# Kernel tuning notes

Hardware: AMD Instinct MI355X
Metric: run time of the kernel (lower is better)

Reference implementation:

```python
import jax, jax.numpy as jnp
import numpy as np

HEADS = 4
DIM_HEAD = 32


def setup_inputs() -> dict:
    key = jax.random.key(0)
    k1, k2, k3, k4 = jax.random.split(key, 4)
    dim = 128
    hidden = HEADS * DIM_HEAD  # 128
    x = jax.random.normal(k1, (32, dim, 64, 64), dtype=jnp.float32)
    w_qkv = jax.random.normal(k2, (3 * hidden, dim), dtype=jnp.float32) * (1.0 / np.sqrt(dim))
    w_out = jax.random.normal(k3, (dim, hidden), dtype=jnp.float32) * (1.0 / np.sqrt(hidden))
    b_out = jax.random.normal(k4, (dim,), dtype=jnp.float32) * 0.01
    return {"x": x, "w_qkv": w_qkv, "w_out": w_out, "b_out": b_out}


def reference(x, w_qkv, w_out, b_out):
    b, c, h, w = x.shape
    n = h * w
    # 1x1 conv (no bias) == channel matmul
    qkv = jnp.einsum('oc,bchw->bohw', w_qkv, x)  # [b, 3*heads*dh, h, w]
    qkv = qkv.reshape(b, 3, HEADS, DIM_HEAD, n)
    q, k, v = qkv[:, 0], qkv[:, 1], qkv[:, 2]  # each [b, heads, dh, n]
    k = jax.nn.softmax(k, axis=-1)  # softmax over spatial positions
    context = jnp.einsum('bhdn,bhen->bhde', k, v)  # [b, heads, dh, dh]
    out = jnp.einsum('bhde,bhdn->bhen', context, q)  # [b, heads, dh, n]
    out = out.reshape(b, HEADS * DIM_HEAD, h, w)
    # 1x1 conv with bias
    return jnp.einsum('oc,bchw->bohw', w_out, out) + b_out[None, :, None, None]
```

## Files before the change

### kernel.cpp

```cpp
#include <hip/hip_runtime.h>
#include <hip/hip_bf16.h>
#include <math.h>

#define BATCH 32
#define CDIM  128
#define NTOT  4096
#define NCH   16
#define CHN   256
#define TN    64

typedef __attribute__((ext_vector_type(4))) float f32x4;
typedef __attribute__((ext_vector_type(8))) short s16x8;

#define PC_OFF  0
#define PC_SIZE (BATCH * 4 * NCH * 32 * 32)
#define PS_OFF  (PC_OFF + PC_SIZE)
#define PS_SIZE (BATCH * 4 * NCH * 32)
#define MBF_OFF (PS_OFF + PS_SIZE)
#define MBF_SIZE (BATCH * CDIM * CDIM / 2)
#define XBT_OFF (MBF_OFF + MBF_SIZE)
#define XBT_SIZE (BATCH * CDIM * NTOT / 2)
#define NEED_BYTES ((size_t)(XBT_OFF + XBT_SIZE) * 4)

static __device__ __forceinline__ unsigned short f2bf(float f) {
    return __builtin_bit_cast(unsigned short, __float2bfloat16(f));
}
static __device__ __forceinline__ unsigned int pack2(float a, float b) {
    return (unsigned int)f2bf(a) | ((unsigned int)f2bf(b) << 16);
}
static __device__ __forceinline__ s16x8 ld_frag_lds(const unsigned int* xsd, int d0) {
    int4 t;
    t.x = (int)xsd[d0]; t.y = (int)xsd[d0 + 1];
    t.z = (int)xsd[d0 + 2]; t.w = (int)xsd[d0 + 3];
    return __builtin_bit_cast(s16x8, t);
}

static __device__ __forceinline__ void stage_xT(const float* __restrict__ xc,
                                                unsigned int* __restrict__ xsd,
                                                int tid) {
    const int m  = tid & 15;
    const int cg = tid >> 4;
#pragma unroll
    for (int p = 0; p < 4; ++p) {
        const int c = 2 * cg + 32 * p;
        const f32x4 a0 = *reinterpret_cast<const f32x4*>(xc + (size_t)c * NTOT + 4 * m);
        const f32x4 a1 = *reinterpret_cast<const f32x4*>(xc + (size_t)(c + 1) * NTOT + 4 * m);
#pragma unroll
        for (int jj = 0; jj < 4; ++jj)
            xsd[(4 * m + jj) * 65 + (c >> 1)] = pack2(a0[jj], a1[jj]);
    }
}

template <bool XBT>
__global__ __launch_bounds__(256, 2)
void k1_ctx(const float* __restrict__ x, const float* __restrict__ wqkv,
            float* __restrict__ ws) {
    __shared__ __attribute__((aligned(16))) unsigned short xsT[64 * 130];
    __shared__ __attribute__((aligned(16))) unsigned short ekv[8][32][72];

    const int j = blockIdx.x, b = blockIdx.y;
    const int tid = threadIdx.x;
    const int l = tid & 63;
    const int w = tid >> 6;
    const int m = l & 15, hq = l >> 4;

    s16x8 afr[4][4];
#pragma unroll
    for (int tm = 0; tm < 4; ++tm)
#pragma unroll
        for (int kt = 0; kt < 4; ++kt) {
            const float* wr = wqkv +
                (size_t)(CDIM + 64 * w + 16 * tm + m) * CDIM + 32 * kt + 8 * hq;
            const f32x4 u0 = *reinterpret_cast<const f32x4*>(wr);
            const f32x4 u1 = *reinterpret_cast<const f32x4*>(wr + 4);
            int4 t4;
            t4.x = (int)pack2(u0[0], u0[1]); t4.y = (int)pack2(u0[2], u0[3]);
            t4.z = (int)pack2(u1[0], u1[1]); t4.w = (int)pack2(u1[2], u1[3]);
            afr[tm][kt] = __builtin_bit_cast(s16x8, t4);
        }

    f32x4 cacc[2][2] = {};
    float sacc[4][4] = {};
    const float* xc = x + (size_t)b * CDIM * NTOT + j * CHN;
    unsigned int* xsd = (unsigned int*)xsT;

    for (int it = 0; it < CHN / TN; ++it) {
        stage_xT(xc + it * TN, xsd, tid);
        __syncthreads();

        if constexpr (XBT) {
            unsigned int* tb = (unsigned int*)(ws + XBT_OFF) +
                               ((size_t)(b * NCH + j) * 4 + it) * 4096;
            const int n = tid >> 2, qt = tid & 3;
#pragma unroll
            for (int p = 0; p < 4; ++p) {
                const int cdl = 16 * p + 4 * qt;
                const int src = n * 65 + (cdl ^ ((n & 7) << 2));
                uint4 v;
                v.x = xsd[src]; v.y = xsd[src + 1];
                v.z = xsd[src + 2]; v.w = xsd[src + 3];
                *reinterpret_cast<uint4*>(tb + (size_t)n * 64 + cdl) = v;
            }
        }

        f32x4 acc[4][4] = {};
#pragma unroll
        for (int kt = 0; kt < 4; ++kt) {
#pragma unroll
            for (int tn = 0; tn < 4; ++tn) {
                const s16x8 bfr = ld_frag_lds(xsd, (16 * tn + m) * 65 + 16 * kt + 4 * hq);
#pragma unroll
                for (int tm = 0; tm < 4; ++tm)
                    acc[tm][tn] = __builtin_amdgcn_mfma_f32_16x16x32_bf16(
                        afr[tm][kt], bfr, acc[tm][tn], 0, 0, 0);
            }
        }

        if (w < 2) {
#pragma unroll
            for (int tm = 0; tm < 4; ++tm)
#pragma unroll
                for (int tn = 0; tn < 4; ++tn)
#pragma unroll
                    for (int r = 0; r < 4; ++r) {
                        const int dg = 64 * w + 16 * tm + 4 * hq + r;
                        const float e = __expf(acc[tm][tn][r]);
                        sacc[tm][r] += e;
                        ekv[dg >> 5][dg & 31][16 * tn + m] = f2bf(e);
                    }
        } else {
#pragma unroll
            for (int tm = 0; tm < 4; ++tm)
#pragma unroll
                for (int tn = 0; tn < 4; ++tn)
#pragma unroll
                    for (int r = 0; r < 4; ++r) {
                        const int eg = 64 * (w - 2) + 16 * tm + 4 * hq + r;
                        ekv[4 + (eg >> 5)][eg & 31][16 * tn + m] = f2bf(acc[tm][tn][r]);
                    }
        }
        __syncthreads();

#pragma unroll
        for (int kt = 0; kt < 2; ++kt) {
            s16x8 va[2], eb[2];
#pragma unroll
            for (int t = 0; t < 2; ++t) {
                va[t] = *reinterpret_cast<const s16x8*>(
                    &ekv[4 + w][16 * t + m][32 * kt + 8 * hq]);
                eb[t] = *reinterpret_cast<const s16x8*>(
                    &ekv[w][16 * t + m][32 * kt + 8 * hq]);
            }
#pragma unroll
            for (int tm = 0; tm < 2; ++tm)
#pragma unroll
                for (int tn = 0; tn < 2; ++tn)
                    cacc[tm][tn] = __builtin_amdgcn_mfma_f32_16x16x32_bf16(
                        va[tm], eb[tn], cacc[tm][tn], 0, 0, 0);
        }
        __syncthreads();
    }

    float* pc = ws + PC_OFF + (size_t)((b * 4 + w) * NCH + j) * 1024;
#pragma unroll
    for (int tm = 0; tm < 2; ++tm)
#pragma unroll
        for (int tn = 0; tn < 2; ++tn)
#pragma unroll
            for (int r = 0; r < 4; ++r)
                pc[(16 * tm + 4 * hq + r) * 32 + 16 * tn + m] = cacc[tm][tn][r];

    if (w < 2) {
#pragma unroll
        for (int tm = 0; tm < 4; ++tm)
#pragma unroll
            for (int r = 0; r < 4; ++r) {
                float s = sacc[tm][r];
                s += __shfl_xor(s, 1);
                s += __shfl_xor(s, 2);
                s += __shfl_xor(s, 4);
                s += __shfl_xor(s, 8);
                if (m == 0) {
                    const int dg = 64 * w + 16 * tm + 4 * hq + r;
                    ws[PS_OFF + (size_t)((b * 4 + (dg >> 5)) * NCH + j) * 32 + (dg & 31)] = s;
                }
            }
    }
}

__global__ __launch_bounds__(256)
void k2_buildM(const float* __restrict__ wqkv, const float* __restrict__ wout,
               float* __restrict__ ws) {
    const int oq = blockIdx.x;
    const int b  = blockIdx.y;
    const int tid = threadIdx.x;

    __shared__ __attribute__((aligned(16))) float smA[8704];
    __shared__ float G[32][133];
    __shared__ float stotS[128];
    float* ctxs  = smA;
    float* wouts = smA + 4224;
    unsigned int* wqs = (unsigned int*)smA;

    if (tid < 128) {
        const int h = tid >> 5, d = tid & 31;
        float s = 0.f;
        for (int j = 0; j < NCH; ++j)
            s += ws[PS_OFF + (size_t)((b * 4 + h) * NCH + j) * 32 + d];
        stotS[tid] = s;
    }
    __syncthreads();

#pragma unroll
    for (int k = 0; k < 16; ++k) {
        const int fid = tid + 256 * k;
        const int h = fid >> 10, rem = fid & 1023;
        const int e = rem >> 5, d = rem & 31;
        float c = 0.f;
        for (int j = 0; j < NCH; ++j)
            c += ws[PC_OFF + (size_t)((b * 4 + h) * NCH + j) * 1024 + rem];
        ctxs[(h * 32 + d) * 33 + e] = c / stotS[h * 32 + d];
    }
#pragma unroll
    for (int k = 0; k < 16; ++k) {
        const int fid = tid + 256 * k;
        const int o = fid >> 7, c = fid & 127;
        wouts[o * 133 + c] = wout[(size_t)(oq * 32 + o) * CDIM + c];
    }
    __syncthreads();

    {
        const int o2 = tid & 31;
        const int g8 = tid >> 5;
#pragma unroll
        for (int i = 0; i < 16; ++i) {
            const int hd = g8 * 16 + i;
            const int h = hd >> 5;
            float acc = 0.f;
#pragma unroll
            for (int e = 0; e < 32; ++e)
                acc = fmaf(wouts[o2 * 133 + h * 32 + e], ctxs[hd * 33 + e], acc);
            G[o2][hd] = acc;
        }
    }
    __syncthreads();

    {
#pragma unroll
        for (int k = 0; k < 32; ++k) {
            const int fid = tid + 256 * k;
            const int hd = fid >> 6, cd = fid & 63;
            const float2 wv =
                *reinterpret_cast<const float2*>(wqkv + (size_t)hd * CDIM + 2 * cd);
            wqs[hd * 68 + cd] = pack2(wv.x, wv.y);
        }
    }
    __syncthreads();

    {
        const int o3 = tid >> 3;
        const int c0 = tid & 7;
        float Macc[16];
#pragma unroll
        for (int i = 0; i < 16; ++i) Macc[i] = 0.f;
        for (int hd = 0; hd < 128; ++hd) {
            const float gv = G[o3][hd];
            const uint4 w0 = *reinterpret_cast<const uint4*>(&wqs[hd * 68 + c0 * 8]);
            const uint4 w1 = *reinterpret_cast<const uint4*>(&wqs[hd * 68 + c0 * 8 + 4]);
            const unsigned int dw[8] = {w0.x, w0.y, w0.z, w0.w, w1.x, w1.y, w1.z, w1.w};
#pragma unroll
            for (int q = 0; q < 8; ++q) {
                const float lo = __builtin_bit_cast(float, dw[q] << 16);
                const float hi = __builtin_bit_cast(float, dw[q] & 0xffff0000u);
                Macc[2 * q]     = fmaf(gv, lo, Macc[2 * q]);
                Macc[2 * q + 1] = fmaf(gv, hi, Macc[2 * q + 1]);
            }
        }
        unsigned int* mpd = (unsigned int*)((unsigned short*)(ws + MBF_OFF) +
                                            (size_t)b * CDIM * CDIM) +
                            (oq * 32 + o3) * 64 + c0 * 8;
        uint4 s0, s1;
        s0.x = pack2(Macc[0], Macc[1]);   s0.y = pack2(Macc[2], Macc[3]);
        s0.z = pack2(Macc[4], Macc[5]);   s0.w = pack2(Macc[6], Macc[7]);
        s1.x = pack2(Macc[8], Macc[9]);   s1.y = pack2(Macc[10], Macc[11]);
        s1.z = pack2(Macc[12], Macc[13]); s1.w = pack2(Macc[14], Macc[15]);
        *reinterpret_cast<uint4*>(mpd) = s0;
        *reinterpret_cast<uint4*>(mpd + 4) = s1;
    }
}

template <bool XBT>
__global__ __launch_bounds__(256)
void k3_final(const float* __restrict__ x, const float* __restrict__ bout,
              const float* __restrict__ ws, float* __restrict__ out) {
    __shared__ __attribute__((aligned(16))) unsigned short xsT[64 * 130];

    const int j = blockIdx.x, b = blockIdx.y;
    const int tid = threadIdx.x, l = tid & 63, w = tid >> 6;
    const int m = l & 15, hq = l >> 4;

    const unsigned short* mbf =
        (const unsigned short*)(ws + MBF_OFF) + (size_t)b * CDIM * CDIM;
    s16x8 afr[2][4];
#pragma unroll
    for (int tm = 0; tm < 2; ++tm)
#pragma unroll
        for (int kt = 0; kt < 4; ++kt)
            afr[tm][kt] = *reinterpret_cast<const s16x8*>(
                mbf + (size_t)(32 * w + 16 * tm + m) * CDIM + 32 * kt + 8 * hq);
    float bias[2][4];
#pragma unroll
    for (int tm = 0; tm < 2; ++tm)
#pragma unroll
        for (int r = 0; r < 4; ++r)
            bias[tm][r] = bout[32 * w + 16 * tm + 4 * hq + r];

    unsigned int* xsd = (unsigned int*)xsT;
    const float* xc = x + (size_t)b * CDIM * NTOT + j * CHN;
    float* oc = out + (size_t)b * CDIM * NTOT + j * CHN;

    for (int it = 0; it < CHN / TN; ++it) {
        if constexpr (XBT) {
            const unsigned int* tb = (const unsigned int*)(ws + XBT_OFF) +
                                     ((size_t)(b * NCH + j) * 4 + it) * 4096;
#pragma unroll
            for (int rep = 0; rep < 4; ++rep) {
                const int dw = rep * 1024 + tid * 4;
                *reinterpret_cast<uint4*>(&xsd[dw]) =
                    *reinterpret_cast<const uint4*>(tb + dw);
            }
        } else {
            stage_xT(xc + it * TN, xsd, tid);
        }
        __syncthreads();

        f32x4 acc[2][4] = {};
#pragma unroll
        for (int kt = 0; kt < 4; ++kt) {
#pragma unroll
            for (int tn = 0; tn < 4; ++tn) {
                const int nl = 16 * tn + m;
                s16x8 bfr;
                if constexpr (XBT) {
                    const int idx = nl * 64 + ((16 * kt + 4 * hq) ^ ((nl & 7) << 2));
                    bfr = __builtin_bit_cast(
                        s16x8, *reinterpret_cast<const int4*>(&xsd[idx]));
                } else {
                    bfr = ld_frag_lds(xsd, nl * 65 + 16 * kt + 4 * hq);
                }
#pragma unroll
                for (int tm = 0; tm < 2; ++tm)
                    acc[tm][tn] = __builtin_amdgcn_mfma_f32_16x16x32_bf16(
                        afr[tm][kt], bfr, acc[tm][tn], 0, 0, 0);
            }
        }
#pragma unroll
        for (int tm = 0; tm < 2; ++tm)
#pragma unroll
            for (int tn = 0; tn < 4; ++tn)
#pragma unroll
                for (int r = 0; r < 4; ++r)
                    oc[(size_t)(32 * w + 16 * tm + 4 * hq + r) * NTOT +
                       it * TN + 16 * tn + m] = acc[tm][tn][r] + bias[tm][r];
        __syncthreads();
    }
}

extern "C" void kernel_launch(void* const* d_in, const int* in_sizes, int n_in,
                              void* d_out, int out_size, void* d_ws, size_t ws_size,
                              hipStream_t stream) {
    const float* x    = (const float*)d_in[0];
    const float* wqkv = (const float*)d_in[1];
    const float* wout = (const float*)d_in[2];
    const float* bout = (const float*)d_in[3];
    float* out = (float*)d_out;
    float* ws  = (float*)d_ws;

    const bool xbt = ws_size >= NEED_BYTES;

    if (xbt)
        k1_ctx<true><<<dim3(NCH, BATCH), 256, 0, stream>>>(x, wqkv, ws);
    else
        k1_ctx<false><<<dim3(NCH, BATCH), 256, 0, stream>>>(x, wqkv, ws);

    k2_buildM<<<dim3(4, BATCH), 256, 0, stream>>>(wqkv, wout, ws);

    if (xbt)
        k3_final<true><<<dim3(NCH, BATCH), 256, 0, stream>>>(x, bout, ws, out);
    else
        k3_final<false><<<dim3(NCH, BATCH), 256, 0, stream>>>(x, bout, ws, out);
}
```

Baseline: 78.05 us.

## Split k1 into finer chunks, prefetch x, separate ctx reduction, async-stage k3

```diff
diff --git a/kernel.cpp b/kernel.cpp
--- a/kernel.cpp
+++ b/kernel.cpp
@@ -5,9 +5,11 @@
 #define BATCH 32
 #define CDIM  128
 #define NTOT  4096
-#define NCH   16
-#define CHN   256
+#define NCH   32
+#define CHN   128
 #define TN    64
+#define NCH3  16
+#define CHN3  256
 
 typedef __attribute__((ext_vector_type(4))) float f32x4;
 typedef __attribute__((ext_vector_type(8))) short s16x8;
@@ -18,7 +20,9 @@
 #define PS_SIZE (BATCH * 4 * NCH * 32)
 #define MBF_OFF (PS_OFF + PS_SIZE)
 #define MBF_SIZE (BATCH * CDIM * CDIM / 2)
-#define XBT_OFF (MBF_OFF + MBF_SIZE)
+#define CTX_OFF (MBF_OFF + MBF_SIZE)
+#define CTX_SIZE (BATCH * 4 * 1024)
+#define XBT_OFF (CTX_OFF + CTX_SIZE)
 #define XBT_SIZE (BATCH * CDIM * NTOT / 2)
 #define NEED_BYTES ((size_t)(XBT_OFF + XBT_SIZE) * 4)
 
@@ -28,10 +32,10 @@
 static __device__ __forceinline__ unsigned int pack2(float a, float b) {
     return (unsigned int)f2bf(a) | ((unsigned int)f2bf(b) << 16);
 }
-static __device__ __forceinline__ s16x8 ld_frag_lds(const unsigned int* xsd, int d0) {
+static __device__ __forceinline__ s16x8 ld_frag_lds(const unsigned int* p, int d0) {
     int4 t;
-    t.x = (int)xsd[d0]; t.y = (int)xsd[d0 + 1];
-    t.z = (int)xsd[d0 + 2]; t.w = (int)xsd[d0 + 3];
+    t.x = (int)p[d0]; t.y = (int)p[d0 + 1];
+    t.z = (int)p[d0 + 2]; t.w = (int)p[d0 + 3];
     return __builtin_bit_cast(s16x8, t);
 }
 
@@ -52,17 +56,18 @@
 }
 
 template <bool XBT>
-__global__ __launch_bounds__(256, 2)
+__global__ __launch_bounds__(256, 3)
 void k1_ctx(const float* __restrict__ x, const float* __restrict__ wqkv,
             float* __restrict__ ws) {
     __shared__ __attribute__((aligned(16))) unsigned short xsT[64 * 130];
-    __shared__ __attribute__((aligned(16))) unsigned short ekv[8][32][72];
+    __shared__ __attribute__((aligned(16))) unsigned short ekv[8 * 32 * 68];
 
     const int j = blockIdx.x, b = blockIdx.y;
     const int tid = threadIdx.x;
     const int l = tid & 63;
     const int w = tid >> 6;
     const int m = l & 15, hq = l >> 4;
+    const int mm = tid & 15, cg = tid >> 4;
 
     s16x8 afr[4][4];
 #pragma unroll
@@ -83,14 +88,50 @@
     float sacc[4][4] = {};
     const float* xc = x + (size_t)b * CDIM * NTOT + j * CHN;
     unsigned int* xsd = (unsigned int*)xsT;
+    unsigned int* ekvd = (unsigned int*)ekv;
+
+    f32x4 xr[8];
+    auto load_x = [&](const float* xp) {
+#pragma unroll
+        for (int p = 0; p < 4; ++p) {
+            const int c = 2 * cg + 32 * p;
+            xr[2 * p]     = *reinterpret_cast<const f32x4*>(xp + (size_t)c * NTOT + 4 * mm);
+            xr[2 * p + 1] = *reinterpret_cast<const f32x4*>(xp + (size_t)(c + 1) * NTOT + 4 * mm);
+        }
+    };
+    auto write_x = [&]() {
+#pragma unroll
+        for (int p = 0; p < 4; ++p) {
+            const int c = 2 * cg + 32 * p;
+#pragma unroll
+            for (int jj = 0; jj < 4; ++jj)
+                xsd[(4 * mm + jj) * 65 + (c >> 1)] = pack2(xr[2 * p][jj], xr[2 * p + 1][jj]);
+        }
+    };
+
+    load_x(xc);
 
     for (int it = 0; it < CHN / TN; ++it) {
-        stage_xT(xc + it * TN, xsd, tid);
+        write_x();
         __syncthreads();
+        if (it + 1 < CHN / TN) load_x(xc + (it + 1) * TN);
+
+        f32x4 acc[4][4] = {};
+#pragma unroll
+        for (int kt = 0; kt < 4; ++kt) {
+#pragma unroll
+            for (int tn = 0; tn < 4; ++tn) {
+                const s16x8 bfr = ld_frag_lds(xsd, (16 * tn + m) * 65 + 16 * kt + 4 * hq);
+#pragma unroll
+                for (int tm = 0; tm < 4; ++tm)
+                    acc[tm][tn] = __builtin_amdgcn_mfma_f32_16x16x32_bf16(
+                        afr[tm][kt], bfr, acc[tm][tn], 0, 0, 0);
+            }
+        }
 
         if constexpr (XBT) {
             unsigned int* tb = (unsigned int*)(ws + XBT_OFF) +
-                               ((size_t)(b * NCH + j) * 4 + it) * 4096;
+                               ((size_t)b * 64 + j * 2 + it) * 4096;
             const int n = tid >> 2, qt = tid & 3;
 #pragma unroll
             for (int p = 0; p < 4; ++p) {
@@ -103,19 +144,6 @@
             }
         }
 
-        f32x4 acc[4][4] = {};
-#pragma unroll
-        for (int kt = 0; kt < 4; ++kt) {
-#pragma unroll
-            for (int tn = 0; tn < 4; ++tn) {
-                const s16x8 bfr = ld_frag_lds(xsd, (16 * tn + m) * 65 + 16 * kt + 4 * hq);
-#pragma unroll
-                for (int tm = 0; tm < 4; ++tm)
-                    acc[tm][tn] = __builtin_amdgcn_mfma_f32_16x16x32_bf16(
-                        afr[tm][kt], bfr, acc[tm][tn], 0, 0, 0);
-            }
-        }
-
         if (w < 2) {
 #pragma unroll
             for (int tm = 0; tm < 4; ++tm)
@@ -126,7 +154,7 @@
                         const int dg = 64 * w + 16 * tm + 4 * hq + r;
                         const float e = __expf(acc[tm][tn][r]);
                         sacc[tm][r] += e;
-                        ekv[dg >> 5][dg & 31][16 * tn + m] = f2bf(e);
+                        ekv[((dg >> 5) * 32 + (dg & 31)) * 68 + 16 * tn + m] = f2bf(e);
                     }
         } else {
 #pragma unroll
@@ -136,7 +164,8 @@
 #pragma unroll
                     for (int r = 0; r < 4; ++r) {
                         const int eg = 64 * (w - 2) + 16 * tm + 4 * hq + r;
-                        ekv[4 + (eg >> 5)][eg & 31][16 * tn + m] = f2bf(acc[tm][tn][r]);
+                        ekv[((4 + (eg >> 5)) * 32 + (eg & 31)) * 68 + 16 * tn + m] =
+                            f2bf(acc[tm][tn][r]);
                     }
         }
         __syncthreads();
@@ -146,10 +175,10 @@
             s16x8 va[2], eb[2];
 #pragma unroll
             for (int t = 0; t < 2; ++t) {
-                va[t] = *reinterpret_cast<const s16x8*>(
-                    &ekv[4 + w][16 * t + m][32 * kt + 8 * hq]);
-                eb[t] = *reinterpret_cast<const s16x8*>(
-                    &ekv[w][16 * t + m][32 * kt + 8 * hq]);
+                va[t] = ld_frag_lds(ekvd,
+                    ((4 + w) * 32 + 16 * t + m) * 34 + 16 * kt + 4 * hq);
+                eb[t] = ld_frag_lds(ekvd,
+                    (w * 32 + 16 * t + m) * 34 + 16 * kt + 4 * hq);
             }
 #pragma unroll
             for (int tm = 0; tm < 2; ++tm)
@@ -158,7 +187,6 @@
                     cacc[tm][tn] = __builtin_amdgcn_mfma_f32_16x16x32_bf16(
                         va[tm], eb[tn], cacc[tm][tn], 0, 0, 0);
         }
-        __syncthreads();
     }
 
     float* pc = ws + PC_OFF + (size_t)((b * 4 + w) * NCH + j) * 1024;
@@ -189,37 +217,46 @@
 }
 
 __global__ __launch_bounds__(256)
-void k2_buildM(const float* __restrict__ wqkv, const float* __restrict__ wout,
-               float* __restrict__ ws) {
+void k2a_ctx(float* __restrict__ ws) {
+    const int bh = blockIdx.x;
+    const int tid = threadIdx.x;
+    __shared__ float stotS[32];
+    if (tid < 32) {
+        float s = 0.f;
+        for (int jj = 0; jj < NCH; ++jj)
+            s += ws[PS_OFF + (size_t)(bh * NCH + jj) * 32 + tid];
+        stotS[tid] = s;
+    }
+    __syncthreads();
+#pragma unroll
+    for (int k = 0; k < 4; ++k) {
+        const int idx = tid + 256 * k;
+        float c = 0.f;
+        for (int jj = 0; jj < NCH; ++jj)
+            c += ws[PC_OFF + (size_t)(bh * NCH + jj) * 1024 + idx];
+        ws[CTX_OFF + (size_t)bh * 1024 + idx] = c / stotS[idx & 31];
+    }
+}
+
+__global__ __launch_bounds__(256)
+void k2b_buildM(const float* __restrict__ wqkv, const float* __restrict__ wout,
+                float* __restrict__ ws) {
     const int oq = blockIdx.x;
     const int b  = blockIdx.y;
     const int tid = threadIdx.x;
 
     __shared__ __attribute__((aligned(16))) float smA[8704];
     __shared__ float G[32][133];
-    __shared__ float stotS[128];
     float* ctxs  = smA;
     float* wouts = smA + 4224;
     unsigned int* wqs = (unsigned int*)smA;
-
-    if (tid < 128) {
-        const int h = tid >> 5, d = tid & 31;
-        float s = 0.f;
-        for (int j = 0; j < NCH; ++j)
-            s += ws[PS_OFF + (size_t)((b * 4 + h) * NCH + j) * 32 + d];
-        stotS[tid] = s;
-    }
-    __syncthreads();
 
 #pragma unroll
     for (int k = 0; k < 16; ++k) {
         const int fid = tid + 256 * k;
         const int h = fid >> 10, rem = fid & 1023;
         const int e = rem >> 5, d = rem & 31;
-        float c = 0.f;
-        for (int j = 0; j < NCH; ++j)
-            c += ws[PC_OFF + (size_t)((b * 4 + h) * NCH + j) * 1024 + rem];
-        ctxs[(h * 32 + d) * 33 + e] = c / stotS[h * 32 + d];
+        ctxs[(h * 32 + d) * 33 + e] = ws[CTX_OFF + (size_t)b * 4096 + fid];
     }
 #pragma unroll
     for (int k = 0; k < 16; ++k) {
@@ -293,7 +330,7 @@
 __global__ __launch_bounds__(256)
 void k3_final(const float* __restrict__ x, const float* __restrict__ bout,
               const float* __restrict__ ws, float* __restrict__ out) {
-    __shared__ __attribute__((aligned(16))) unsigned short xsT[64 * 130];
+    __shared__ __attribute__((aligned(16))) unsigned int xs2[2][4160];
 
     const int j = blockIdx.x, b = blockIdx.y;
     const int tid = threadIdx.x, l = tid & 63, w = tid >> 6;
@@ -315,25 +352,37 @@
         for (int r = 0; r < 4; ++r)
             bias[tm][r] = bout[32 * w + 16 * tm + 4 * hq + r];
 
-    unsigned int* xsd = (unsigned int*)xsT;
-    const float* xc = x + (size_t)b * CDIM * NTOT + j * CHN;
-    float* oc = out + (size_t)b * CDIM * NTOT + j * CHN;
-
-    for (int it = 0; it < CHN / TN; ++it) {
+    const float* xc = x + (size_t)b * CDIM * NTOT + j * CHN3;
+    float* oc = out + (size_t)b * CDIM * NTOT + j * CHN3;
+    const unsigned int* tb = (const unsigned int*)(ws + XBT_OFF) +
+                             ((size_t)b * 64 + j * 4) * 4096;
+
+    auto stage_async = [&](const unsigned int* src, unsigned int* dstbase) {
+        unsigned int* dst = dstbase + (tid >> 6) * 256;
+        const unsigned int* s = src + tid * 4;
+#pragma unroll
+        for (int rep = 0; rep < 4; ++rep) {
+            __builtin_amdgcn_global_load_lds(
+                (const __attribute__((address_space(1))) unsigned int*)(s + rep * 1024),
+                (__attribute__((address_space(3))) unsigned int*)(dst + rep * 1024),
+                16, 0, 0);
+        }
+    };
+
+    int cur = 0;
+    if constexpr (XBT) stage_async(tb, xs2[0]);
+
+    for (int it = 0; it < 4; ++it) {
         if constexpr (XBT) {
-            const unsigned int* tb = (const unsigned int*)(ws + XBT_OFF) +
-                                     ((size_t)(b * NCH + j) * 4 + it) * 4096;
-#pragma unroll
-            for (int rep = 0; rep < 4; ++rep) {
-                const int dw = rep * 1024 + tid * 4;
-                *reinterpret_cast<uint4*>(&xsd[dw]) =
-                    *reinterpret_cast<const uint4*>(tb + dw);
-            }
+            __syncthreads();
+            if (it < 3) stage_async(tb + (it + 1) * 4096, xs2[cur ^ 1]);
         } else {
-            stage_xT(xc + it * TN, xsd, tid);
-        }
-        __syncthreads();
-
+            __syncthreads();
+            stage_xT(xc + it * TN, xs2[cur], tid);
+            __syncthreads();
+        }
+
+        const unsigned int* buf = xs2[cur];
         f32x4 acc[2][4] = {};
 #pragma unroll
         for (int kt = 0; kt < 4; ++kt) {
@@ -344,9 +393,9 @@
                 if constexpr (XBT) {
                     const int idx = nl * 64 + ((16 * kt + 4 * hq) ^ ((nl & 7) << 2));
                     bfr = __builtin_bit_cast(
-                        s16x8, *reinterpret_cast<const int4*>(&xsd[idx]));
+                        s16x8, *reinterpret_cast<const int4*>(&buf[idx]));
                 } else {
-                    bfr = ld_frag_lds(xsd, nl * 65 + 16 * kt + 4 * hq);
+                    bfr = ld_frag_lds(buf, nl * 65 + 16 * kt + 4 * hq);
                 }
 #pragma unroll
                 for (int tm = 0; tm < 2; ++tm)
@@ -362,7 +411,7 @@
                 for (int r = 0; r < 4; ++r)
                     oc[(size_t)(32 * w + 16 * tm + 4 * hq + r) * NTOT +
                        it * TN + 16 * tn + m] = acc[tm][tn][r] + bias[tm][r];
-        __syncthreads();
+        cur ^= 1;
     }
 }
 
@@ -383,10 +432,11 @@
     else
         k1_ctx<false><<<dim3(NCH, BATCH), 256, 0, stream>>>(x, wqkv, ws);
 
-    k2_buildM<<<dim3(4, BATCH), 256, 0, stream>>>(wqkv, wout, ws);
+    k2a_ctx<<<BATCH * 4, 256, 0, stream>>>(ws);
+    k2b_buildM<<<dim3(4, BATCH), 256, 0, stream>>>(wqkv, wout, ws);
 
     if (xbt)
-        k3_final<true><<<dim3(NCH, BATCH), 256, 0, stream>>>(x, bout, ws, out);
+        k3_final<true><<<dim3(NCH3, BATCH), 256, 0, stream>>>(x, bout, ws, out);
     else
-        k3_final<false><<<dim3(NCH, BATCH), 256, 0, stream>>>(x, bout, ws, out);
-}
+        k3_final<false><<<dim3(NCH3, BATCH), 256, 0, stream>>>(x, bout, ws, out);
+}
```

Result: slower. 168.5 us (+115.9%).
